# Kernel tuning notes

Hardware: AMD Instinct MI355X
Metric: run time of the kernel (lower is better)

## Reference

```python
import jax, jax.numpy as jnp
import numpy as np

B, T, D = 128, 1024, 1024


def setup_inputs() -> dict:
    key = jax.random.key(0)
    ks = jax.random.split(key, 6)
    s = 0.02  # small init scale for weights
    return {
        "z_eeg": jax.random.normal(ks[0], (B, T, D), dtype=jnp.float32),
        "z_rppg": jax.random.normal(ks[1], (B, D), dtype=jnp.float32),
        "Wq": jax.random.normal(ks[2], (D, D), dtype=jnp.float32) * s,
        "Wk": jax.random.normal(ks[3], (D, D), dtype=jnp.float32) * s,
        "Wm_w": jax.random.normal(ks[4], (D, D), dtype=jnp.float32) * s,
        "Wm_b": jnp.zeros((D,), dtype=jnp.float32),
        "Wf_w": jax.random.normal(ks[5], (2 * D, D), dtype=jnp.float32) * s,
        "Wf_b": jnp.zeros((D,), dtype=jnp.float32),
        "bf": jnp.zeros((D,), dtype=jnp.float32),
    }


def reference(z_eeg, z_rppg, Wq, Wk, Wm_w, Wm_b, Wf_w, Wf_b, bf):
    d = Wq.shape[-1]
    Q = z_rppg @ Wq                                    # [B, D]
    K = jnp.einsum("btd,de->bte", z_eeg, Wk)          # [B, T, D]
    scores = jnp.einsum("bd,btd->bt", Q, K) / jnp.sqrt(jnp.float32(d))  # [B, T]
    w = jax.nn.softmax(scores, axis=1)                 # [B, T]
    A = jnp.einsum("bt,btd->bd", w, z_eeg)            # attention-pooled EEG [B, D]
    concat = jnp.concatenate([A, z_rppg], axis=-1)     # [B, 2D]
    f = jax.nn.sigmoid(concat @ Wf_w + Wf_b + bf)      # gate [B, D]
    m = A @ Wm_w + Wm_b                                # [B, D]
    h = jax.nn.relu(z_rppg + m * f)                    # gated residual fusion
    return h
```

## Files before the change

kernel.cpp:

```cpp
#include <hip/hip_runtime.h>
#include <hip/hip_bf16.h>


#define BB   128
#define TT   1024
#define DD   1024
#define NT   16
#define KS   8
#define QS   4

__global__ __launch_bounds__(256) void k_gemm_ab(const float* __restrict__ X,
                                                 const float* __restrict__ W,
                                                 float* __restrict__ Cpart) {
  const int t = threadIdx.x;
  const int ebase = blockIdx.x * 64;
  const int bbase = blockIdx.y * 16;
  const int p = blockIdx.z;
  const int e = ebase + (t & 63);
  const int bg = t >> 6;
  __shared__ __align__(16) float Xs[16][64];
  float acc[4] = {0.f, 0.f, 0.f, 0.f};
  const int kend = p * 256 + 256;
  for (int k0 = p * 256; k0 < kend; k0 += 64) {
#pragma unroll
    for (int j = 0; j < 4; ++j) {
      int i = t + 256 * j;
      Xs[i >> 6][i & 63] = X[(size_t)(bbase + (i >> 6)) * DD + k0 + (i & 63)];
    }
    __syncthreads();
#pragma unroll 16
    for (int kk = 0; kk < 64; ++kk) {
      float w = W[(size_t)(k0 + kk) * DD + e];
#pragma unroll
      for (int j = 0; j < 4; ++j) acc[j] = fmaf(Xs[bg + 4 * j][kk], w, acc[j]);
    }
    __syncthreads();
  }
#pragma unroll
  for (int j = 0; j < 4; ++j)
    Cpart[(size_t)p * BB * DD + (size_t)(bbase + bg + 4 * j) * DD + e] = acc[j];
}

__global__ __launch_bounds__(256) void k_gemm_abt(const float* __restrict__ Qpart,
                                                  const float* __restrict__ W,
                                                  float* __restrict__ Cpart) {
  const int t = threadIdx.x;
  const int dbase = blockIdx.x * 64;
  const int bbase = blockIdx.y * 16;
  const int p = blockIdx.z;
  const int dl = t & 63;
  const int bg = t >> 6;
  __shared__ __align__(16) float Xs[16][64];
  __shared__ __align__(16) float Ws[64][65];
  float acc[4] = {0.f, 0.f, 0.f, 0.f};
  const int kend = p * 256 + 256;
  for (int k0 = p * 256; k0 < kend; k0 += 64) {
#pragma unroll
    for (int j = 0; j < 4; ++j) {
      int i = t + 256 * j;
      const size_t base = (size_t)(bbase + (i >> 6)) * DD + k0 + (i & 63);
      float v = Qpart[base] + Qpart[base + (size_t)BB * DD] +
                Qpart[base + 2 * (size_t)BB * DD] + Qpart[base + 3 * (size_t)BB * DD];
      Xs[i >> 6][i & 63] = v;
    }
#pragma unroll
    for (int j = 0; j < 16; ++j) {
      int i = t + 256 * j;
      Ws[i >> 6][i & 63] = W[(size_t)(dbase + (i >> 6)) * DD + k0 + (i & 63)];
    }
    __syncthreads();
#pragma unroll 8
    for (int kk = 0; kk < 64; ++kk) {
      float w = Ws[dl][kk];
#pragma unroll
      for (int j = 0; j < 4; ++j) acc[j] = fmaf(Xs[bg + 4 * j][kk], w, acc[j]);
    }
    __syncthreads();
  }
#pragma unroll
  for (int j = 0; j < 4; ++j)
    Cpart[(size_t)p * BB * DD + (size_t)(bbase + bg + 4 * j) * DD + dbase + dl] = acc[j];
}

__global__ __launch_bounds__(256) void k_attn(const float* __restrict__ z_eeg,
                                              const float* __restrict__ Qkpart,
                                              float* __restrict__ Npart,
                                              float* __restrict__ Zpart) {
  const int t = threadIdx.x;
  const int lane = t & 63;
  const int w = t >> 6;
  const int tblk = blockIdx.x;
  const int b = blockIdx.y;

  float4 qk4[4];
#pragma unroll
  for (int q = 0; q < 4; ++q) {
    const float4* p0 = (const float4*)(Qkpart + (size_t)b * DD);
    float4 a = p0[q * 64 + lane];
#pragma unroll
    for (int pp = 1; pp < QS; ++pp) {
      float4 s = ((const float4*)(Qkpart + (size_t)pp * BB * DD + (size_t)b * DD))[q * 64 + lane];
      a.x += s.x; a.y += s.y; a.z += s.z; a.w += s.w;
    }
    a.x *= 0.03125f; a.y *= 0.03125f; a.z *= 0.03125f; a.w *= 0.03125f;
    qk4[q] = a;
  }

  float4 acc[4] = {};
  float zsum = 0.f;
  const float4* zb = (const float4*)(z_eeg + (size_t)b * TT * DD);
  const int row0 = tblk * (TT / NT) + w;

  for (int i = 0; i < 8; ++i) {
    const int rA = row0 + i * 8;
    const int rB = rA + 4;
    const float4* zpA = zb + (size_t)rA * (DD / 4);
    const float4* zpB = zb + (size_t)rB * (DD / 4);
    float4 zA[4], zB[4];
#pragma unroll
    for (int q = 0; q < 4; ++q) zA[q] = zpA[q * 64 + lane];
#pragma unroll
    for (int q = 0; q < 4; ++q) zB[q] = zpB[q * 64 + lane];
    float dotA = 0.f, dotB = 0.f;
#pragma unroll
    for (int q = 0; q < 4; ++q) {
      dotA += zA[q].x * qk4[q].x + zA[q].y * qk4[q].y + zA[q].z * qk4[q].z + zA[q].w * qk4[q].w;
      dotB += zB[q].x * qk4[q].x + zB[q].y * qk4[q].y + zB[q].z * qk4[q].z + zB[q].w * qk4[q].w;
    }
#pragma unroll
    for (int off = 32; off >= 1; off >>= 1) {
      dotA += __shfl_xor(dotA, off);
      dotB += __shfl_xor(dotB, off);
    }
    const float eA = __expf(dotA);
    const float eB = __expf(dotB);
    zsum += eA + eB;
#pragma unroll
    for (int q = 0; q < 4; ++q) {
      acc[q].x = fmaf(eA, zA[q].x, acc[q].x);
      acc[q].y = fmaf(eA, zA[q].y, acc[q].y);
      acc[q].z = fmaf(eA, zA[q].z, acc[q].z);
      acc[q].w = fmaf(eA, zA[q].w, acc[q].w);
      acc[q].x = fmaf(eB, zB[q].x, acc[q].x);
      acc[q].y = fmaf(eB, zB[q].y, acc[q].y);
      acc[q].z = fmaf(eB, zB[q].z, acc[q].z);
      acc[q].w = fmaf(eB, zB[q].w, acc[q].w);
    }
  }

  __shared__ __align__(16) float4 sacc[3][256];
  __shared__ float szw[4];
  if (w > 0) {
#pragma unroll
    for (int q = 0; q < 4; ++q) sacc[w - 1][q * 64 + lane] = acc[q];
  }
  if (lane == 0) szw[w] = zsum;
  __syncthreads();
  if (w == 0) {
    float4* np = (float4*)(Npart + ((size_t)b * NT + tblk) * DD);
#pragma unroll
    for (int q = 0; q < 4; ++q) {
      float4 a = acc[q];
#pragma unroll
      for (int ww = 0; ww < 3; ++ww) {
        float4 s = sacc[ww][q * 64 + lane];
        a.x += s.x; a.y += s.y; a.z += s.z; a.w += s.w;
      }
      np[q * 64 + lane] = a;
    }
    if (lane == 0) Zpart[b * NT + tblk] = szw[0] + szw[1] + szw[2] + szw[3];
  }
}

__global__ __launch_bounds__(256) void k_reduce_a(const float* __restrict__ Npart,
                                                  const float* __restrict__ Zpart,
                                                  float* __restrict__ A) {
  const int idx = blockIdx.x * 256 + threadIdx.x;
  const int b = idx >> 10;
  const int d = idx & 1023;
  float n = 0.f, z = 0.f;
#pragma unroll
  for (int k = 0; k < NT; ++k) {
    n += Npart[((size_t)b * NT + k) * DD + d];
    z += Zpart[b * NT + k];
  }
  A[idx] = n / z;
}

__device__ __forceinline__ void outer_acc(float4 acc[4], const float4 a, const float4 w) {
  acc[0].x = fmaf(a.x, w.x, acc[0].x); acc[0].y = fmaf(a.x, w.y, acc[0].y);
  acc[0].z = fmaf(a.x, w.z, acc[0].z); acc[0].w = fmaf(a.x, w.w, acc[0].w);
  acc[1].x = fmaf(a.y, w.x, acc[1].x); acc[1].y = fmaf(a.y, w.y, acc[1].y);
  acc[1].z = fmaf(a.y, w.z, acc[1].z); acc[1].w = fmaf(a.y, w.w, acc[1].w);
  acc[2].x = fmaf(a.z, w.x, acc[2].x); acc[2].y = fmaf(a.z, w.y, acc[2].y);
  acc[2].z = fmaf(a.z, w.z, acc[2].z); acc[2].w = fmaf(a.z, w.w, acc[2].w);
  acc[3].x = fmaf(a.w, w.x, acc[3].x); acc[3].y = fmaf(a.w, w.y, acc[3].y);
  acc[3].z = fmaf(a.w, w.z, acc[3].z); acc[3].w = fmaf(a.w, w.w, acc[3].w);
}

__global__ __launch_bounds__(256) void k_epi_partial(const float* __restrict__ A,
                                                     const float* __restrict__ z_rppg,
                                                     const float* __restrict__ Wf_w,
                                                     const float* __restrict__ Wm_w,
                                                     float* __restrict__ fpart,
                                                     float* __restrict__ mpart) {
  const int t = threadIdx.x;
  const int dbase = blockIdx.x * 32;
  const int ks = blockIdx.y;
  const int bq = t >> 3;
  const int dg = t & 7;
  __shared__ __align__(16) float Cst[32][132];
  __shared__ __align__(16) float Ws[32][36];
  float4 accf[4] = {};
  float4 accm[4] = {};

  {
    const float* src = (ks < 4) ? (A + ks * 256) : (z_rppg + ks * 256 - 1024);
    const float* wsrc = Wf_w + (size_t)ks * 256 * DD;
    for (int k0 = 0; k0 < 256; k0 += 32) {
#pragma unroll
      for (int j = 0; j < 16; ++j) {
        int i = t + 256 * j; int bb = i >> 5, c = i & 31;
        Cst[c][bb] = src[(size_t)bb * DD + k0 + c];
      }
#pragma unroll
      for (int j = 0; j < 4; ++j) {
        int i = t + 256 * j; int r = i >> 5, c = i & 31;
        Ws[r][c] = wsrc[(size_t)(k0 + r) * DD + dbase + c];
      }
      __syncthreads();
#pragma unroll
      for (int kk = 0; kk < 32; ++kk) {
        float4 a4 = *(const float4*)&Cst[kk][bq * 4];
        float4 w4 = *(const float4*)&Ws[kk][dg * 4];
        outer_acc(accf, a4, w4);
      }
      __syncthreads();
    }
  }
  {
    const float* src = A + ks * 128;
    const float* wsrc = Wm_w + (size_t)ks * 128 * DD;
    for (int k0 = 0; k0 < 128; k0 += 32) {
#pragma unroll
      for (int j = 0; j < 16; ++j) {
        int i = t + 256 * j; int bb = i >> 5, c = i & 31;
        Cst[c][bb] = src[(size_t)bb * DD + k0 + c];
      }
#pragma unroll
      for (int j = 0; j < 4; ++j) {
        int i = t + 256 * j; int r = i >> 5, c = i & 31;
        Ws[r][c] = wsrc[(size_t)(k0 + r) * DD + dbase + c];
      }
      __syncthreads();
#pragma unroll
      for (int kk = 0; kk < 32; ++kk) {
        float4 a4 = *(const float4*)&Cst[kk][bq * 4];
        float4 w4 = *(const float4*)&Ws[kk][dg * 4];
        outer_acc(accm, a4, w4);
      }
      __syncthreads();
    }
  }
#pragma unroll
  for (int i = 0; i < 4; ++i) {
    const int b = bq * 4 + i;
    *(float4*)&fpart[(size_t)ks * (BB * DD) + (size_t)b * DD + dbase + dg * 4] = accf[i];
    *(float4*)&mpart[(size_t)ks * (BB * DD) + (size_t)b * DD + dbase + dg * 4] = accm[i];
  }
}

__global__ __launch_bounds__(256) void k_combine(const float* __restrict__ fpart,
                                                 const float* __restrict__ mpart,
                                                 const float* __restrict__ Wf_b,
                                                 const float* __restrict__ bf,
                                                 const float* __restrict__ Wm_b,
                                                 const float* __restrict__ z_rppg,
                                                 float* __restrict__ out) {
  const int idx = blockIdx.x * 256 + threadIdx.x;
  const int d = idx & 1023;
  float f = Wf_b[d] + bf[d];
  float m = Wm_b[d];
#pragma unroll
  for (int k = 0; k < KS; ++k) {
    f += fpart[(size_t)k * (BB * DD) + idx];
    m += mpart[(size_t)k * (BB * DD) + idx];
  }
  const float g = 1.f / (1.f + __expf(-f));
  const float h = z_rppg[idx] + m * g;
  out[idx] = h > 0.f ? h : 0.f;
}

extern "C" void kernel_launch(void* const* d_in, const int* in_sizes, int n_in,
                              void* d_out, int out_size, void* d_ws, size_t ws_size,
                              hipStream_t stream) {
  const float* z_eeg  = (const float*)d_in[0];
  const float* z_rppg = (const float*)d_in[1];
  const float* Wq     = (const float*)d_in[2];
  const float* Wk     = (const float*)d_in[3];
  const float* Wm_w   = (const float*)d_in[4];
  const float* Wm_b   = (const float*)d_in[5];
  const float* Wf_w   = (const float*)d_in[6];
  const float* Wf_b   = (const float*)d_in[7];
  const float* bf     = (const float*)d_in[8];
  float* out = (float*)d_out;

  float* ws = (float*)d_ws;
  float* Qpart  = ws;
  float* Qkpart = Qpart + (size_t)QS * BB * DD;
  float* Npart  = Qkpart + (size_t)QS * BB * DD;
  float* Zpart  = Npart + (size_t)BB * NT * DD;
  float* A      = Zpart + BB * NT;
  float* fpart  = Npart;
  float* mpart  = Npart + (size_t)KS * BB * DD;

  k_gemm_ab<<<dim3(16, 8, QS), 256, 0, stream>>>(z_rppg, Wq, Qpart);
  k_gemm_abt<<<dim3(16, 8, QS), 256, 0, stream>>>(Qpart, Wk, Qkpart);
  k_attn<<<dim3(NT, BB), 256, 0, stream>>>(z_eeg, Qkpart, Npart, Zpart);
  k_reduce_a<<<(BB * DD) / 256, 256, 0, stream>>>(Npart, Zpart, A);
  k_epi_partial<<<dim3(32, KS), 256, 0, stream>>>(A, z_rppg, Wf_w, Wm_w, fpart, mpart);
  k_combine<<<(BB * DD) / 256, 256, 0, stream>>>(fpart, mpart, Wf_b, bf, Wm_b, z_rppg, out);
}
```

Baseline: 216.9 us.

## Raise epilogue split-K to 32 and software-prefetch z_eeg rows in attention

The epilogue GEMM split-K factor goes from 8 to 32, so k_epi_partial launches 4x more blocks, each with a shorter K range. This fills more CUs at the cost of much larger fpart/mpart partial buffers, now placed after A, and more reduction work in k_combine. The attention kernel also double-buffers z_eeg row loads in registers, issuing the next rows' loads before computing on the current ones to hide memory latency. The prefetch raises register pressure.

```diff
diff --git a/kernel.cpp b/kernel.cpp
--- a/kernel.cpp
+++ b/kernel.cpp
@@ -6,7 +6,7 @@
 #define TT   1024
 #define DD   1024
 #define NT   16
-#define KS   8
+#define KS   32
 #define QS   4
 
 __global__ __launch_bounds__(256) void k_gemm_ab(const float* __restrict__ X,
@@ -95,11 +95,10 @@
   float4 qk4[4];
 #pragma unroll
   for (int q = 0; q < 4; ++q) {
-    const float4* p0 = (const float4*)(Qkpart + (size_t)b * DD);
-    float4 a = p0[q * 64 + lane];
+    float4 a = ((const float4*)(Qkpart + (size_t)b * DD))[q * 64 + lane];
 #pragma unroll
     for (int pp = 1; pp < QS; ++pp) {
-      float4 s = ((const float4*)(Qkpart + (size_t)pp * BB * DD + (size_t)b * DD))[q * 64 + lane];
+      float4 s = ((const float4*)(Qkpart + ((size_t)pp * BB + b) * DD))[q * 64 + lane];
       a.x += s.x; a.y += s.y; a.z += s.z; a.w += s.w;
     }
     a.x *= 0.03125f; a.y *= 0.03125f; a.z *= 0.03125f; a.w *= 0.03125f;
@@ -109,23 +108,33 @@
   float4 acc[4] = {};
   float zsum = 0.f;
   const float4* zb = (const float4*)(z_eeg + (size_t)b * TT * DD);
-  const int row0 = tblk * (TT / NT) + w;
-
+  const int row0 = tblk * 64 + w;
+
+  float4 cA[4], cB[4];
+  {
+    const float4* pA = zb + (size_t)row0 * 256;
+    const float4* pB = zb + (size_t)(row0 + 4) * 256;
+#pragma unroll
+    for (int q = 0; q < 4; ++q) cA[q] = pA[q * 64 + lane];
+#pragma unroll
+    for (int q = 0; q < 4; ++q) cB[q] = pB[q * 64 + lane];
+  }
+#pragma unroll
   for (int i = 0; i < 8; ++i) {
-    const int rA = row0 + i * 8;
-    const int rB = rA + 4;
-    const float4* zpA = zb + (size_t)rA * (DD / 4);
-    const float4* zpB = zb + (size_t)rB * (DD / 4);
-    float4 zA[4], zB[4];
-#pragma unroll
-    for (int q = 0; q < 4; ++q) zA[q] = zpA[q * 64 + lane];
-#pragma unroll
-    for (int q = 0; q < 4; ++q) zB[q] = zpB[q * 64 + lane];
+    float4 nA[4], nB[4];
+    if (i < 7) {
+      const float4* pA = zb + (size_t)(row0 + (i + 1) * 8) * 256;
+      const float4* pB = zb + (size_t)(row0 + (i + 1) * 8 + 4) * 256;
+#pragma unroll
+      for (int q = 0; q < 4; ++q) nA[q] = pA[q * 64 + lane];
+#pragma unroll
+      for (int q = 0; q < 4; ++q) nB[q] = pB[q * 64 + lane];
+    }
     float dotA = 0.f, dotB = 0.f;
 #pragma unroll
     for (int q = 0; q < 4; ++q) {
-      dotA += zA[q].x * qk4[q].x + zA[q].y * qk4[q].y + zA[q].z * qk4[q].z + zA[q].w * qk4[q].w;
-      dotB += zB[q].x * qk4[q].x + zB[q].y * qk4[q].y + zB[q].z * qk4[q].z + zB[q].w * qk4[q].w;
+      dotA += cA[q].x * qk4[q].x + cA[q].y * qk4[q].y + cA[q].z * qk4[q].z + cA[q].w * qk4[q].w;
+      dotB += cB[q].x * qk4[q].x + cB[q].y * qk4[q].y + cB[q].z * qk4[q].z + cB[q].w * qk4[q].w;
     }
 #pragma unroll
     for (int off = 32; off >= 1; off >>= 1) {
@@ -137,14 +146,18 @@
     zsum += eA + eB;
 #pragma unroll
     for (int q = 0; q < 4; ++q) {
-      acc[q].x = fmaf(eA, zA[q].x, acc[q].x);
-      acc[q].y = fmaf(eA, zA[q].y, acc[q].y);
-      acc[q].z = fmaf(eA, zA[q].z, acc[q].z);
-      acc[q].w = fmaf(eA, zA[q].w, acc[q].w);
-      acc[q].x = fmaf(eB, zB[q].x, acc[q].x);
-      acc[q].y = fmaf(eB, zB[q].y, acc[q].y);
-      acc[q].z = fmaf(eB, zB[q].z, acc[q].z);
-      acc[q].w = fmaf(eB, zB[q].w, acc[q].w);
+      acc[q].x = fmaf(eA, cA[q].x, acc[q].x);
+      acc[q].y = fmaf(eA, cA[q].y, acc[q].y);
+      acc[q].z = fmaf(eA, cA[q].z, acc[q].z);
+      acc[q].w = fmaf(eA, cA[q].w, acc[q].w);
+      acc[q].x = fmaf(eB, cB[q].x, acc[q].x);
+      acc[q].y = fmaf(eB, cB[q].y, acc[q].y);
+      acc[q].z = fmaf(eB, cB[q].z, acc[q].z);
+      acc[q].w = fmaf(eB, cB[q].w, acc[q].w);
+    }
+    if (i < 7) {
+#pragma unroll
+      for (int q = 0; q < 4; ++q) { cA[q] = nA[q]; cB[q] = nB[q]; }
     }
   }
 
@@ -215,9 +228,9 @@
   float4 accm[4] = {};
 
   {
-    const float* src = (ks < 4) ? (A + ks * 256) : (z_rppg + ks * 256 - 1024);
-    const float* wsrc = Wf_w + (size_t)ks * 256 * DD;
-    for (int k0 = 0; k0 < 256; k0 += 32) {
+    const float* src = (ks < 16) ? (A + ks * 64) : (z_rppg + ks * 64 - 1024);
+    const float* wsrc = Wf_w + (size_t)ks * 64 * DD;
+    for (int k0 = 0; k0 < 64; k0 += 32) {
 #pragma unroll
       for (int j = 0; j < 16; ++j) {
         int i = t + 256 * j; int bb = i >> 5, c = i & 31;
@@ -239,27 +252,24 @@
     }
   }
   {
-    const float* src = A + ks * 128;
-    const float* wsrc = Wm_w + (size_t)ks * 128 * DD;
-    for (int k0 = 0; k0 < 128; k0 += 32) {
-#pragma unroll
-      for (int j = 0; j < 16; ++j) {
-        int i = t + 256 * j; int bb = i >> 5, c = i & 31;
-        Cst[c][bb] = src[(size_t)bb * DD + k0 + c];
-      }
-#pragma unroll
-      for (int j = 0; j < 4; ++j) {
-        int i = t + 256 * j; int r = i >> 5, c = i & 31;
-        Ws[r][c] = wsrc[(size_t)(k0 + r) * DD + dbase + c];
-      }
-      __syncthreads();
-#pragma unroll
-      for (int kk = 0; kk < 32; ++kk) {
-        float4 a4 = *(const float4*)&Cst[kk][bq * 4];
-        float4 w4 = *(const float4*)&Ws[kk][dg * 4];
-        outer_acc(accm, a4, w4);
-      }
-      __syncthreads();
+    const float* src = A + ks * 32;
+    const float* wsrc = Wm_w + (size_t)ks * 32 * DD;
+#pragma unroll
+    for (int j = 0; j < 16; ++j) {
+      int i = t + 256 * j; int bb = i >> 5, c = i & 31;
+      Cst[c][bb] = src[(size_t)bb * DD + c];
+    }
+#pragma unroll
+    for (int j = 0; j < 4; ++j) {
+      int i = t + 256 * j; int r = i >> 5, c = i & 31;
+      Ws[r][c] = wsrc[(size_t)r * DD + dbase + c];
+    }
+    __syncthreads();
+#pragma unroll
+    for (int kk = 0; kk < 32; ++kk) {
+      float4 a4 = *(const float4*)&Cst[kk][bq * 4];
+      float4 w4 = *(const float4*)&Ws[kk][dg * 4];
+      outer_acc(accm, a4, w4);
     }
   }
 #pragma unroll
@@ -311,8 +321,8 @@
   float* Npart  = Qkpart + (size_t)QS * BB * DD;
   float* Zpart  = Npart + (size_t)BB * NT * DD;
   float* A      = Zpart + BB * NT;
-  float* fpart  = Npart;
-  float* mpart  = Npart + (size_t)KS * BB * DD;
+  float* fpart  = A + (size_t)BB * DD;
+  float* mpart  = fpart + (size_t)KS * BB * DD;
 
   k_gemm_ab<<<dim3(16, 8, QS), 256, 0, stream>>>(z_rppg, Wq, Qpart);
   k_gemm_abt<<<dim3(16, 8, QS), 256, 0, stream>>>(Qpart, Wk, Qkpart);
```

Measured after the change: 225.9 us. 4.1% more time.
